# Kernel tuning notes

Hardware: AMD Instinct MI355X
Metric: run time of the kernel (lower is better)

## Reference

```python
import jax, jax.numpy as jnp
import numpy as np
from jax.scipy.special import logsumexp

B, S, H, T, M = 64, 512, 768, 500, 8
POSITION_WEIGHT = 0.6
LABEL_SMOOTH = 0.1
GAMMA = 2.0


def setup_inputs() -> dict:
    key = jax.random.key(0)
    ks = jax.random.split(key, 12)
    hidden = jax.random.normal(ks[0], (B, S, H), jnp.float32)  # BERT sequence_output stand-in
    lengths = jax.random.randint(ks[1], (B,), S // 2, S + 1)
    attention_mask = (jnp.arange(S)[None, :] < lengths[:, None]).astype(jnp.int32)
    position_labels = jax.random.randint(ks[2], (B, S), 0, 3).astype(jnp.int32)
    type_labels = jax.random.randint(ks[3], (B, M), 0, T).astype(jnp.int32)
    starts = jax.random.randint(ks[4], (B, M), 1, S // 2)
    ends = starts + jax.random.randint(ks[5], (B, M), 2, 8)
    valid = jax.random.uniform(ks[6], (B, M)) < 0.8  # some (batch, span) slots unused, like the original sum()>0 filter
    target_positions = jnp.where(valid[..., None], jnp.stack([starts, ends], -1), 0).astype(jnp.int32)
    # CRF params exactly as hardcoded in __init__
    trans = jnp.array([[-5.0, 20.0, -10000.0], [-50.0, 0.0, 50.0], [0.0, -50.0, 30.0]], jnp.float32)
    start_trans = jnp.array([0.0, 0.0, -10000.0], jnp.float32)
    end_trans = jnp.array([0.0, -100.0, 0.0], jnp.float32)
    return {
        'hidden': hidden,
        'attention_mask': attention_mask,
        'position_labels': position_labels,
        'type_labels': type_labels,
        'target_positions': target_positions,
        'bi_label_weight': jnp.asarray(0.5, jnp.float32),
        'W_pos': 0.02 * jax.random.normal(ks[7], (H, 3), jnp.float32),
        'b_pos': jnp.zeros((3,), jnp.float32),
        'start_trans': start_trans,
        'end_trans': end_trans,
        'trans': trans,
        'att_W1': 0.02 * jax.random.normal(ks[8], (H, 64), jnp.float32),
        'att_b1': jnp.zeros((64,), jnp.float32),
        'att_W2': 0.02 * jax.random.normal(ks[9], (64, 1), jnp.float32),
        'att_b2': jnp.zeros((1,), jnp.float32),
        'W_type': 0.02 * jax.random.normal(ks[10], (H, T), jnp.float32),
        'b_type': jnp.zeros((T,), jnp.float32),
    }


def crf_nll(em, labels, mask, start_trans, end_trans, trans):
    # torchcrf-style masked negative log-likelihood, reduction='none'
    maskf = mask.astype(em.dtype)
    emit = jnp.take_along_axis(em, labels[..., None], -1)[..., 0]  # [B,S]
    emit_score = (emit * maskf).sum(1)
    tr = trans[labels[:, :-1], labels[:, 1:]]  # [B,S-1]
    tr_score = (tr * maskf[:, 1:]).sum(1)
    last = mask.sum(1) - 1
    last_tags = jnp.take_along_axis(labels, last[:, None], 1)[:, 0]
    score = start_trans[labels[:, 0]] + emit_score + tr_score + end_trans[last_tags]
    # log partition via scan over time
    alpha = start_trans[None, :] + em[:, 0]  # [B,3]
    def step(alpha, xs):
        em_t, m_t = xs
        nxt = logsumexp(alpha[:, :, None] + trans[None, :, :] + em_t[:, None, :], axis=1)
        return jnp.where(m_t[:, None], nxt, alpha), None
    alpha, _ = jax.lax.scan(step, alpha, (em[:, 1:].transpose(1, 0, 2), mask[:, 1:].T))
    logZ = logsumexp(alpha + end_trans[None, :], axis=-1)
    return logZ - score  # = -log_likelihood


def reference(hidden, attention_mask, position_labels, type_labels, target_positions,
              bi_label_weight, W_pos, b_pos, start_trans, end_trans, trans,
              att_W1, att_b1, att_W2, att_b2, W_type, b_type):
    mask = attention_mask.astype(bool)
    emissions = hidden @ W_pos + b_pos  # [B,S,3]
    w = jnp.where(position_labels > 0, 1.0 + bi_label_weight, 1.0)[..., None]
    em_w = emissions * w
    position_loss = crf_nll(em_w, position_labels, mask, start_trans, end_trans, trans).mean()

    # span attention pooling, batched over all (B,M) pairs instead of the Python loop
    scores = (jnp.tanh(hidden @ att_W1 + att_b1) @ att_W2 + att_b2)[..., 0]  # [B,S]
    starts = target_positions[..., 0]
    ends = target_positions[..., 1]
    valid = target_positions.sum(-1) > 0  # [B,M]
    pos = jnp.arange(hidden.shape[1])
    span_mask = (pos[None, None, :] >= starts[..., None]) & (pos[None, None, :] < ends[..., None])  # [B,M,S]
    att = jnp.where(span_mask, scores[:, None, :], -1e9)
    aw = jax.nn.softmax(att, axis=-1)  # per-span softmax == softmax over the gathered span
    pooled = jnp.einsum('bms,bsh->bmh', aw, hidden)  # [B,M,H]
    logits = pooled @ W_type + b_type  # [B,M,T]

    # label-smoothed focal loss over valid spans only
    nT = logits.shape[-1]
    onehot = jax.nn.one_hot(type_labels, nT, dtype=logits.dtype)
    smooth = onehot * (1.0 - LABEL_SMOOTH) + LABEL_SMOOTH / nT
    logp = jax.nn.log_softmax(logits, axis=-1)
    probs = jnp.exp(logp)
    ce = -(smooth * logp).sum(-1)
    pt = (smooth * probs).sum(-1)
    focal = ce * (1.0 - pt) ** GAMMA
    v = valid.astype(focal.dtype)
    type_loss = (focal * v).sum() / jnp.maximum(v.sum(), 1.0) * 10.0

    joint = POSITION_WEIGHT * position_loss + (1.0 - POSITION_WEIGHT) * type_loss
    return jnp.stack([joint, position_loss, type_loss])
```

## Files before the change

### kernel.cpp

```cpp
#include <hip/hip_runtime.h>

#define L2E 1.44269504088896340736f
#define LN2 0.69314718055994530942f
#define NEGB -1e30f

typedef float f32x4 __attribute__((ext_vector_type(4)));
typedef __bf16 bf16x8 __attribute__((ext_vector_type(8)));

static constexpr int NB = 64, NS = 512, NH = 768, NT = 500, NM = 8;

static constexpr size_t WT_ALL_OFF   = 0;
static constexpr size_t WT_TYPE_OFF  = 122880;
static constexpr size_t EM_T_OFF     = 909312;
static constexpr size_t SCORES_OFF   = 1302528;
static constexpr size_t LABELS_T_OFF = 1433600;
static constexpr size_t LEN_OFF      = 1564672;
static constexpr size_t SCAL_OFF     = 3399936;
static constexpr size_t MATM_OFF     = 3400192;
static constexpr size_t PSC_OFF      = 3547648;

__device__ __forceinline__ unsigned short f2bf(float f) {
  unsigned u = __builtin_bit_cast(unsigned, f);
  u += 0x7FFFu + ((u >> 16) & 1u);
  return (unsigned short)(u >> 16);
}
__device__ __forceinline__ float sel3(float a, float b, float c, int i) {
  return i == 0 ? a : (i == 1 ? b : c);
}
__device__ __forceinline__ float lse3(float x, float y, float z) {
  float m = fmaxf(fmaxf(x, y), z);
  float p = exp2f((x - m) * L2E) + exp2f((y - m) * L2E) + exp2f((z - m) * L2E);
  return m + log2f(p) * LN2;
}
__device__ __forceinline__ int swz(int row, int slot) {
  return row * 128 + ((slot ^ (row & 7)) << 4);
}

__global__ __launch_bounds__(256) void ka_prep(
    const float* __restrict__ W1, const float* __restrict__ Wpos,
    const float* __restrict__ Wtype, const int* __restrict__ amask,
    unsigned short* __restrict__ wt_all, unsigned short* __restrict__ wt_type,
    int* __restrict__ lengths, float* __restrict__ scal) {
  const int bid = blockIdx.x, t = threadIdx.x;
  if (bid < 108) {
    __shared__ float tl[64][65];
    const bool is_type = bid < 96;
    const int kt = is_type ? (bid % 12) : (bid - 96);
    const int k0 = kt * 64;
    const int n0 = is_type ? (bid / 12) * 64 : 0;
    const int ld = is_type ? 500 : 64;
    const int nlim = is_type ? 500 : 64;
    const float* src = is_type ? Wtype : W1;
    unsigned short* dst = is_type ? wt_type : wt_all;
    const int n = t & 63;
    #pragma unroll
    for (int i = 0; i < 16; ++i) {
      int k = i * 4 + (t >> 6);
      tl[k][n] = (n0 + n < nlim) ? src[(size_t)(k0 + k) * ld + n0 + n] : 0.f;
    }
    __syncthreads();
    const int k = t & 63;
    #pragma unroll
    for (int i = 0; i < 16; ++i) {
      int nn = i * 4 + (t >> 6);
      dst[(size_t)(n0 + nn) * 768 + k0 + k] = f2bf(tl[k][nn]);
    }
  } else if (bid == 108) {
    for (int idx = t; idx < 16 * 768; idx += 256) {
      int n = 64 + idx / 768, k = idx % 768;
      float v = (n < 67) ? Wpos[k * 3 + (n - 64)] : 0.f;
      wt_all[(size_t)n * 768 + k] = f2bf(v);
    }
  } else {
    __shared__ int part[256];
    int bb = t >> 2, qq = t & 3;
    const int4* mp = (const int4*)(amask + bb * 512 + qq * 128);
    int s = 0;
    #pragma unroll 8
    for (int i = 0; i < 32; ++i) { int4 v = mp[i]; s += v.x + v.y + v.z + v.w; }
    part[t] = s;
    __syncthreads();
    if (qq == 0) lengths[bb] = part[t] + part[t + 1] + part[t + 2] + part[t + 3];
    if (t == 0) { scal[1] = 0.f; scal[2] = 0.f; }
  }
}

__global__ __launch_bounds__(256) void k1_gemm(
    const float* __restrict__ hidden, const int* __restrict__ plab,
    const float* __restrict__ bpos, const float* __restrict__ b1,
    const float* __restrict__ W2, const float* __restrict__ b2,
    const float* __restrict__ biw, const unsigned short* __restrict__ wt_all,
    float* __restrict__ em_t, float* __restrict__ scores, int* __restrict__ labels_t) {
  __shared__ char lds[8192 + 10240];
  char* As = lds;
  char* Bs = lds + 8192;
  const int t = threadIdx.x, w = t >> 6, l = t & 63;
  const int row0 = blockIdx.x * 64;

  f32x4 acc[5];
  #pragma unroll
  for (int nt = 0; nt < 5; ++nt) acc[nt] = (f32x4){0.f, 0.f, 0.f, 0.f};

  auto loadAB = [&](int it, float4 av[4], uint4 bv[3]) {
    const int k0 = it * 64;
    #pragma unroll
    for (int u = 0; u < 4; ++u) {
      int f4 = t + 256 * u, r = f4 >> 4, k4 = f4 & 15;
      av[u] = *(const float4*)(hidden + (size_t)(row0 + r) * 768 + k0 + 4 * k4);
    }
    bv[0] = *(const uint4*)(wt_all + (t >> 3) * 768 + k0 + 8 * (t & 7));
    bv[1] = *(const uint4*)(wt_all + ((t + 256) >> 3) * 768 + k0 + 8 * (t & 7));
    bv[2] = (t < 128) ? *(const uint4*)(wt_all + ((t + 512) >> 3) * 768 + k0 + 8 * (t & 7))
                      : (uint4){0, 0, 0, 0};
  };

  float4 avc[4]; uint4 bvc[3];
  loadAB(0, avc, bvc);

  for (int it = 0; it < 12; ++it) {
    __syncthreads();
    #pragma unroll
    for (int u = 0; u < 4; ++u) {
      int f4 = t + 256 * u, r = f4 >> 4, k4 = f4 & 15;
      unsigned lo = (unsigned)f2bf(avc[u].x) | ((unsigned)f2bf(avc[u].y) << 16);
      unsigned hi = (unsigned)f2bf(avc[u].z) | ((unsigned)f2bf(avc[u].w) << 16);
      int byte = r * 128 + (((k4 >> 1) ^ (r & 7)) << 4) + (k4 & 1) * 8;
      *(uint2*)(As + byte) = make_uint2(lo, hi);
    }
    { int n = t >> 3, kc = t & 7;         *(uint4*)(Bs + swz(n, kc)) = bvc[0]; }
    { int n = (t + 256) >> 3, kc = t & 7; *(uint4*)(Bs + swz(n, kc)) = bvc[1]; }
    if (t < 128) { int n = (t + 512) >> 3, kc = t & 7; *(uint4*)(Bs + swz(n, kc)) = bvc[2]; }
    __syncthreads();

    float4 avn[4]; uint4 bvn[3];
    if (it < 11) loadAB(it + 1, avn, bvn);

    #pragma unroll
    for (int ks = 0; ks < 2; ++ks) {
      int arow = 16 * w + (l & 15);
      int slot = 4 * ks + (l >> 4);
      bf16x8 a = *(const bf16x8*)(As + swz(arow, slot));
      #pragma unroll
      for (int nt = 0; nt < 5; ++nt) {
        int brow = 16 * nt + (l & 15);
        bf16x8 b = *(const bf16x8*)(Bs + swz(brow, slot));
        acc[nt] = __builtin_amdgcn_mfma_f32_16x16x32_bf16(a, b, acc[nt], 0, 0, 0);
      }
    }
    if (it < 11) {
      #pragma unroll
      for (int u = 0; u < 4; ++u) avc[u] = avn[u];
      #pragma unroll
      for (int u = 0; u < 3; ++u) bvc[u] = bvn[u];
    }
  }

  const int q = l >> 4, c16 = l & 15;
  const float bias2 = b2[0];
  #pragma unroll
  for (int r = 0; r < 4; ++r) {
    float s = 0.f;
    #pragma unroll
    for (int nt = 0; nt < 4; ++nt) {
      int c = 16 * nt + c16;
      float x = acc[nt][r] + b1[c];
      float th = 1.f - 2.f / (1.f + exp2f(x * (2.f * L2E)));
      s += th * W2[c];
    }
    #pragma unroll
    for (int off = 1; off < 16; off <<= 1) s += __shfl_xor(s, off, 64);
    if (c16 == 0) {
      int row = row0 + 16 * w + 4 * q + r;
      scores[row] = s + bias2;
    }
  }
  if (c16 < 3) {
    const float bi = biw[0];
    #pragma unroll
    for (int r = 0; r < 4; ++r) {
      int row = row0 + 16 * w + 4 * q + r;
      int bb = row >> 9, ss = row & 511;
      int lab = plab[row];
      float wgt = (lab > 0) ? 1.f + bi : 1.f;
      float ev = (acc[4][r] + bpos[c16]) * wgt;
      em_t[(ss * 3 + c16) * 64 + bb] = ev;
      if (c16 == 0) labels_t[ss * 64 + bb] = lab;
    }
  }
}

__global__ __launch_bounds__(64) void k2a_chunk(
    const float* __restrict__ em_t, const int* __restrict__ labels_t,
    const int* __restrict__ lengths, const float* __restrict__ trans,
    float* __restrict__ matM, float* __restrict__ psc) {
  const int b = threadIdx.x, c = blockIdx.x;
  float T0 = trans[0], T1 = trans[1], T2 = trans[2];
  float T3 = trans[3], T4 = trans[4], T5 = trans[5];
  float T6 = trans[6], T7 = trans[7], T8 = trans[8];
  const int L = lengths[b];
  const int s0 = 8 * c;
  int labp = labels_t[(c ? (s0 - 1) : 0) * 64 + b];

  float E0[8], E1[8], E2[8]; int LB[8];
  #pragma unroll
  for (int i = 0; i < 8; ++i) {
    E0[i] = em_t[((s0 + i) * 3 + 0) * 64 + b];
    E1[i] = em_t[((s0 + i) * 3 + 1) * 64 + b];
    E2[i] = em_t[((s0 + i) * 3 + 2) * 64 + b];
    LB[i] = labels_t[(s0 + i) * 64 + b];
  }

  float M[9];
  #pragma unroll
  for (int i = 0; i < 9; ++i) M[i] = (i == 0 || i == 4 || i == 8) ? 0.f : NEGB;
  float sc = 0.f;

  #pragma unroll
  for (int i = 0; i < 8; ++i) {
    int s = s0 + i;
    bool act = (s >= 1) && (s < L);
    float N[9];
    #pragma unroll
    for (int r = 0; r < 3; ++r) {
      float ma = M[3 * r], mb = M[3 * r + 1], mc = M[3 * r + 2];
      N[3 * r + 0] = lse3(ma + T0, mb + T3, mc + T6) + E0[i];
      N[3 * r + 1] = lse3(ma + T1, mb + T4, mc + T7) + E1[i];
      N[3 * r + 2] = lse3(ma + T2, mb + T5, mc + T8) + E2[i];
    }
    #pragma unroll
    for (int r = 0; r < 9; ++r) M[r] = act ? N[r] : M[r];
    int lab = LB[i];
    float ev = sel3(E0[i], E1[i], E2[i], lab);
    float trv = sel3(sel3(T0, T1, T2, lab),
                     sel3(T3, T4, T5, lab),
                     sel3(T6, T7, T8, lab), labp);
    sc += act ? (ev + trv) : 0.f;
    labp = lab;
  }
  #pragma unroll
  for (int i = 0; i < 9; ++i) matM[(c * 9 + i) * 64 + b] = M[i];
  psc[c * 64 + b] = sc;
}

__global__ __launch_bounds__(256) void kd_pool_gemm_focal(
    const float* __restrict__ hidden, const float* __restrict__ scores,
    const int* __restrict__ tpos, const int* __restrict__ tlab,
    const unsigned short* __restrict__ wt_type, const float* __restrict__ btype,
    float* __restrict__ scal) {
  __shared__ unsigned short Apool[8][776];
  __shared__ float red[4][8][3];
  __shared__ float vl[8];
  const int t = threadIdx.x, w = t >> 6, l = t & 63;
  const int b = blockIdx.x;

  {
    const int sp = t >> 5;
    const int span = b * 8 + sp;
    const int st = tpos[span * 2], en = tpos[span * 2 + 1];
    const int len = (st + en > 0) ? (en - st) : 0;
    float sv[7], aw[7];
    float wm = -1e30f;
    #pragma unroll
    for (int j = 0; j < 7; ++j) {
      sv[j] = (j < len) ? scores[b * 512 + st + j] : -1e30f;
      wm = fmaxf(wm, sv[j]);
    }
    float den = 0.f;
    #pragma unroll
    for (int j = 0; j < 7; ++j) {
      aw[j] = (j < len) ? exp2f((sv[j] - wm) * L2E) : 0.f;
      den += aw[j];
    }
    float inv = (den > 0.f) ? 1.f / den : 0.f;
    #pragma unroll
    for (int j = 0; j < 7; ++j) aw[j] *= inv;

    const int h0 = (t & 31) * 24;
    float ap[24];
    #pragma unroll
    for (int i = 0; i < 24; ++i) ap[i] = 0.f;
    #pragma unroll
    for (int j = 0; j < 7; ++j) {
      if (j < len) {
        const float4* hp = (const float4*)(hidden + (size_t)(b * 512 + st + j) * 768 + h0);
        #pragma unroll
        for (int i = 0; i < 6; ++i) {
          float4 v = hp[i];
          ap[4 * i + 0] += aw[j] * v.x; ap[4 * i + 1] += aw[j] * v.y;
          ap[4 * i + 2] += aw[j] * v.z; ap[4 * i + 3] += aw[j] * v.w;
        }
      }
    }
    unsigned short* dp = &Apool[sp][h0];
    #pragma unroll
    for (int g = 0; g < 3; ++g) {
      uint4 v;
      v.x = (unsigned)f2bf(ap[8 * g + 0]) | ((unsigned)f2bf(ap[8 * g + 1]) << 16);
      v.y = (unsigned)f2bf(ap[8 * g + 2]) | ((unsigned)f2bf(ap[8 * g + 3]) << 16);
      v.z = (unsigned)f2bf(ap[8 * g + 4]) | ((unsigned)f2bf(ap[8 * g + 5]) << 16);
      v.w = (unsigned)f2bf(ap[8 * g + 6]) | ((unsigned)f2bf(ap[8 * g + 7]) << 16);
      *(uint4*)(dp + 8 * g) = v;
    }
  }
  __syncthreads();

  f32x4 acc[8];
  #pragma unroll
  for (int nt = 0; nt < 8; ++nt) acc[nt] = (f32x4){0.f, 0.f, 0.f, 0.f};
  const int arow = l & 15;
  const bf16x8 zerov = (bf16x8)(__bf16)0.f;
  for (int ks = 0; ks < 24; ++ks) {
    bf16x8 a = (arow < 8) ? *(const bf16x8*)(&Apool[arow][ks * 32 + 8 * (l >> 4)]) : zerov;
    #pragma unroll
    for (int nt = 0; nt < 8; ++nt) {
      int col = 128 * w + 16 * nt + (l & 15);
      bf16x8 bb = *(const bf16x8*)(wt_type + (size_t)col * 768 + ks * 32 + 8 * (l >> 4));
      acc[nt] = __builtin_amdgcn_mfma_f32_16x16x32_bf16(a, bb, acc[nt], 0, 0, 0);
    }
  }

  float bt[8]; bool vc[8];
  #pragma unroll
  for (int nt = 0; nt < 8; ++nt) {
    int col = 128 * w + 16 * nt + (l & 15);
    vc[nt] = col < 500;
    bt[nt] = vc[nt] ? btype[col] : 0.f;
  }
  #pragma unroll
  for (int r = 0; r < 4; ++r) {
    float lmax = -1e30f, ssum = 0.f;
    #pragma unroll
    for (int nt = 0; nt < 8; ++nt) {
      float lv = vc[nt] ? (acc[nt][r] + bt[nt]) : -1e30f;
      lmax = fmaxf(lmax, lv);
      ssum += vc[nt] ? lv : 0.f;
    }
    #pragma unroll
    for (int off = 1; off < 16; off <<= 1) lmax = fmaxf(lmax, __shfl_xor(lmax, off, 64));
    float sexp = 0.f;
    #pragma unroll
    for (int nt = 0; nt < 8; ++nt) {
      float lv = vc[nt] ? (acc[nt][r] + bt[nt]) : -1e30f;
      sexp += vc[nt] ? exp2f((lv - lmax) * L2E) : 0.f;
    }
    #pragma unroll
    for (int off = 1; off < 16; off <<= 1) {
      sexp += __shfl_xor(sexp, off, 64);
      ssum += __shfl_xor(ssum, off, 64);
    }
    if ((l & 15) == 0 && (l >> 4) < 2) {
      int row = 4 * (l >> 4) + r;
      red[w][row][0] = lmax; red[w][row][1] = sexp; red[w][row][2] = ssum;
    }
    if ((l >> 4) < 2) {
      int row = 4 * (l >> 4) + r;
      int lbl = tlab[b * 8 + row];
      if ((lbl >> 7) == w && (lbl & 15) == (l & 15)) {
        #pragma unroll
        for (int nt = 0; nt < 8; ++nt)
          if (((lbl >> 4) & 7) == nt) vl[row] = acc[nt][r] + btype[lbl];
      }
    }
  }
  __syncthreads();

  float fv = 0.f, vv = 0.f;
  if (t < 8) {
    const int row = t;
    float gm = fmaxf(fmaxf(red[0][row][0], red[1][row][0]),
                     fmaxf(red[2][row][0], red[3][row][0]));
    float sexp = 0.f, ssum = 0.f;
    #pragma unroll
    for (int i = 0; i < 4; ++i) {
      sexp += red[i][row][1] * exp2f((red[i][row][0] - gm) * L2E);
      ssum += red[i][row][2];
    }
    float logZ = gm + log2f(sexp) * LN2;
    float lp = vl[row] - logZ;
    float ce = -(0.9f * lp + 2e-4f * (ssum - 500.f * logZ));
    float pt = 0.9f * exp2f(lp * L2E) + 2e-4f;
    float focal = ce * (1.f - pt) * (1.f - pt);
    int span = b * 8 + row;
    bool valid = (tpos[span * 2] + tpos[span * 2 + 1]) > 0;
    fv = valid ? focal : 0.f;
    vv = valid ? 1.f : 0.f;
  }
  #pragma unroll
  for (int off = 1; off < 8; off <<= 1) {
    fv += __shfl_xor(fv, off, 64);
    vv += __shfl_xor(vv, off, 64);
  }
  if (t == 0) {
    atomicAdd(&scal[1], fv);
    atomicAdd(&scal[2], vv);
  }
}

__global__ __launch_bounds__(64) void k_final(
    const float* __restrict__ em_t, const int* __restrict__ labels_t,
    const int* __restrict__ lengths, const float* __restrict__ strans,
    const float* __restrict__ etrans, const float* __restrict__ matM,
    const float* __restrict__ psc, const float* __restrict__ scal,
    float* __restrict__ out) {
  const int b = threadIdx.x;
  const int L = lengths[b];
  const float st0 = strans[0], st1 = strans[1], st2 = strans[2];
  const float et0 = etrans[0], et1 = etrans[1], et2 = etrans[2];
  float e00 = em_t[0 * 64 + b], e01 = em_t[1 * 64 + b], e02 = em_t[2 * 64 + b];
  int lab0 = labels_t[b];
  float a0 = st0 + e00, a1 = st1 + e01, a2 = st2 + e02;
  float score = sel3(st0, st1, st2, lab0) + sel3(e00, e01, e02, lab0);

  float cur[4][10];
  #pragma unroll
  for (int j = 0; j < 4; ++j) {
    #pragma unroll
    for (int i = 0; i < 9; ++i) cur[j][i] = matM[(j * 9 + i) * 64 + b];
    cur[j][9] = psc[j * 64 + b];
  }

  for (int r = 0; r < 16; ++r) {
    float nxt[4][10];
    if (r < 15) {
      #pragma unroll
      for (int j = 0; j < 4; ++j) {
        int c = (r + 1) * 4 + j;
        #pragma unroll
        for (int i = 0; i < 9; ++i) nxt[j][i] = matM[(c * 9 + i) * 64 + b];
        nxt[j][9] = psc[c * 64 + b];
      }
    }
    #pragma unroll
    for (int j = 0; j < 4; ++j) {
      float n0 = lse3(a0 + cur[j][0], a1 + cur[j][3], a2 + cur[j][6]);
      float n1 = lse3(a0 + cur[j][1], a1 + cur[j][4], a2 + cur[j][7]);
      float n2 = lse3(a0 + cur[j][2], a1 + cur[j][5], a2 + cur[j][8]);
      a0 = n0; a1 = n1; a2 = n2;
      score += cur[j][9];
    }
    if (r < 15) {
      #pragma unroll
      for (int j = 0; j < 4; ++j)
        #pragma unroll
        for (int i = 0; i < 10; ++i) cur[j][i] = nxt[j][i];
    }
  }

  int last = labels_t[(L - 1) * 64 + b];
  score += sel3(et0, et1, et2, last);
  float logZ = lse3(a0 + et0, a1 + et1, a2 + et2);
  float nll = logZ - score;
  #pragma unroll
  for (int off = 1; off < 64; off <<= 1) nll += __shfl_xor(nll, off, 64);
  if (b == 0) {
    float pos = nll / 64.f;
    float type = scal[1] / fmaxf(scal[2], 1.f) * 10.f;
    out[0] = 0.6f * pos + 0.4f * type;
    out[1] = pos;
    out[2] = type;
  }
}

extern "C" void kernel_launch(void* const* d_in, const int* in_sizes, int n_in,
                              void* d_out, int out_size, void* d_ws, size_t ws_size,
                              hipStream_t stream) {
  const float* hidden = (const float*)d_in[0];
  const int*   amask  = (const int*)d_in[1];
  const int*   plab   = (const int*)d_in[2];
  const int*   tlab   = (const int*)d_in[3];
  const int*   tpos   = (const int*)d_in[4];
  const float* biw    = (const float*)d_in[5];
  const float* Wpos   = (const float*)d_in[6];
  const float* bpos   = (const float*)d_in[7];
  const float* strans = (const float*)d_in[8];
  const float* etrans = (const float*)d_in[9];
  const float* trans  = (const float*)d_in[10];
  const float* W1     = (const float*)d_in[11];
  const float* b1     = (const float*)d_in[12];
  const float* W2     = (const float*)d_in[13];
  const float* b2     = (const float*)d_in[14];
  const float* Wtype  = (const float*)d_in[15];
  const float* btype  = (const float*)d_in[16];
  float* out = (float*)d_out;
  char* ws = (char*)d_ws;

  unsigned short* wt_all  = (unsigned short*)(ws + WT_ALL_OFF);
  unsigned short* wt_type = (unsigned short*)(ws + WT_TYPE_OFF);
  float* em_t    = (float*)(ws + EM_T_OFF);
  float* scores  = (float*)(ws + SCORES_OFF);
  int*   labelsT = (int*)(ws + LABELS_T_OFF);
  int*   lengths = (int*)(ws + LEN_OFF);
  float* scal    = (float*)(ws + SCAL_OFF);
  float* matM    = (float*)(ws + MATM_OFF);
  float* psc     = (float*)(ws + PSC_OFF);

  ka_prep<<<110, 256, 0, stream>>>(W1, Wpos, Wtype, amask, wt_all, wt_type, lengths, scal);
  k1_gemm<<<512, 256, 0, stream>>>(hidden, plab, bpos, b1, W2, b2, biw, wt_all,
                                   em_t, scores, labelsT);
  k2a_chunk<<<64, 64, 0, stream>>>(em_t, labelsT, lengths, trans, matM, psc);
  kd_pool_gemm_focal<<<64, 256, 0, stream>>>(hidden, scores, tpos, tlab, wt_type, btype, scal);
  k_final<<<1, 64, 0, stream>>>(em_t, labelsT, lengths, strans, etrans, matM, psc, scal, out);
}
```

Baseline: 104.2 us.

## Drop LDS staging in projection GEMM and fuse CRF chunk with pooling kernel

The hidden-state projection GEMM no longer stages A and B tiles through shared memory with barriers. Each lane now loads its MFMA fragments straight from global memory, converting fp32 to bf16 in registers. Separately, the CRF chunk kernel and the span-pooling/focal kernel are merged into one launch of 80 blocks, with 16 extra blocks running the CRF chunks four waves each, which removes one kernel launch and lets the two run concurrently. The direct global loads give up the LDS data sharing across waves and the prefetch of the next tile, so weight fragments are re-read per wave and latency may be less hidden.

```diff
diff --git a/kernel.cpp b/kernel.cpp
--- a/kernel.cpp
+++ b/kernel.cpp
@@ -32,8 +32,13 @@
   float p = exp2f((x - m) * L2E) + exp2f((y - m) * L2E) + exp2f((z - m) * L2E);
   return m + log2f(p) * LN2;
 }
-__device__ __forceinline__ int swz(int row, int slot) {
-  return row * 128 + ((slot ^ (row & 7)) << 4);
+__device__ __forceinline__ bf16x8 pack8(float4 lo, float4 hi) {
+  union { unsigned u[4]; bf16x8 v; } r;
+  r.u[0] = (unsigned)f2bf(lo.x) | ((unsigned)f2bf(lo.y) << 16);
+  r.u[1] = (unsigned)f2bf(lo.z) | ((unsigned)f2bf(lo.w) << 16);
+  r.u[2] = (unsigned)f2bf(hi.x) | ((unsigned)f2bf(hi.y) << 16);
+  r.u[3] = (unsigned)f2bf(hi.z) | ((unsigned)f2bf(hi.w) << 16);
+  return r.v;
 }
 
 __global__ __launch_bounds__(256) void ka_prep(
@@ -91,71 +96,41 @@
     const float* __restrict__ W2, const float* __restrict__ b2,
     const float* __restrict__ biw, const unsigned short* __restrict__ wt_all,
     float* __restrict__ em_t, float* __restrict__ scores, int* __restrict__ labels_t) {
-  __shared__ char lds[8192 + 10240];
-  char* As = lds;
-  char* Bs = lds + 8192;
   const int t = threadIdx.x, w = t >> 6, l = t & 63;
   const int row0 = blockIdx.x * 64;
+  const int c16 = l & 15, q = l >> 4;
+  const float* aptr = hidden + (size_t)(row0 + 16 * w + c16) * 768;
 
   f32x4 acc[5];
   #pragma unroll
   for (int nt = 0; nt < 5; ++nt) acc[nt] = (f32x4){0.f, 0.f, 0.f, 0.f};
 
-  auto loadAB = [&](int it, float4 av[4], uint4 bv[3]) {
+  #pragma unroll 2
+  for (int it = 0; it < 12; ++it) {
     const int k0 = it * 64;
-    #pragma unroll
-    for (int u = 0; u < 4; ++u) {
-      int f4 = t + 256 * u, r = f4 >> 4, k4 = f4 & 15;
-      av[u] = *(const float4*)(hidden + (size_t)(row0 + r) * 768 + k0 + 4 * k4);
-    }
-    bv[0] = *(const uint4*)(wt_all + (t >> 3) * 768 + k0 + 8 * (t & 7));
-    bv[1] = *(const uint4*)(wt_all + ((t + 256) >> 3) * 768 + k0 + 8 * (t & 7));
-    bv[2] = (t < 128) ? *(const uint4*)(wt_all + ((t + 512) >> 3) * 768 + k0 + 8 * (t & 7))
-                      : (uint4){0, 0, 0, 0};
-  };
-
-  float4 avc[4]; uint4 bvc[3];
-  loadAB(0, avc, bvc);
-
-  for (int it = 0; it < 12; ++it) {
-    __syncthreads();
-    #pragma unroll
-    for (int u = 0; u < 4; ++u) {
-      int f4 = t + 256 * u, r = f4 >> 4, k4 = f4 & 15;
-      unsigned lo = (unsigned)f2bf(avc[u].x) | ((unsigned)f2bf(avc[u].y) << 16);
-      unsigned hi = (unsigned)f2bf(avc[u].z) | ((unsigned)f2bf(avc[u].w) << 16);
-      int byte = r * 128 + (((k4 >> 1) ^ (r & 7)) << 4) + (k4 & 1) * 8;
-      *(uint2*)(As + byte) = make_uint2(lo, hi);
-    }
-    { int n = t >> 3, kc = t & 7;         *(uint4*)(Bs + swz(n, kc)) = bvc[0]; }
-    { int n = (t + 256) >> 3, kc = t & 7; *(uint4*)(Bs + swz(n, kc)) = bvc[1]; }
-    if (t < 128) { int n = (t + 512) >> 3, kc = t & 7; *(uint4*)(Bs + swz(n, kc)) = bvc[2]; }
-    __syncthreads();
-
-    float4 avn[4]; uint4 bvn[3];
-    if (it < 11) loadAB(it + 1, avn, bvn);
-
-    #pragma unroll
-    for (int ks = 0; ks < 2; ++ks) {
-      int arow = 16 * w + (l & 15);
-      int slot = 4 * ks + (l >> 4);
-      bf16x8 a = *(const bf16x8*)(As + swz(arow, slot));
-      #pragma unroll
-      for (int nt = 0; nt < 5; ++nt) {
-        int brow = 16 * nt + (l & 15);
-        bf16x8 b = *(const bf16x8*)(Bs + swz(brow, slot));
-        acc[nt] = __builtin_amdgcn_mfma_f32_16x16x32_bf16(a, b, acc[nt], 0, 0, 0);
-      }
-    }
-    if (it < 11) {
-      #pragma unroll
-      for (int u = 0; u < 4; ++u) avc[u] = avn[u];
-      #pragma unroll
-      for (int u = 0; u < 3; ++u) bvc[u] = bvn[u];
-    }
-  }
-
-  const int q = l >> 4, c16 = l & 15;
+    const int ka0 = k0 + q * 8;
+    const int ka1 = k0 + (4 + q) * 8;
+    float4 a0lo = *(const float4*)(aptr + ka0);
+    float4 a0hi = *(const float4*)(aptr + ka0 + 4);
+    float4 a1lo = *(const float4*)(aptr + ka1);
+    float4 a1hi = *(const float4*)(aptr + ka1 + 4);
+    bf16x8 bf[2][5];
+    #pragma unroll
+    for (int nt = 0; nt < 5; ++nt) {
+      const unsigned short* bp = wt_all + (size_t)(16 * nt + c16) * 768;
+      bf[0][nt] = *(const bf16x8*)(bp + ka0);
+      bf[1][nt] = *(const bf16x8*)(bp + ka1);
+    }
+    bf16x8 a0 = pack8(a0lo, a0hi);
+    bf16x8 a1 = pack8(a1lo, a1hi);
+    #pragma unroll
+    for (int nt = 0; nt < 5; ++nt)
+      acc[nt] = __builtin_amdgcn_mfma_f32_16x16x32_bf16(a0, bf[0][nt], acc[nt], 0, 0, 0);
+    #pragma unroll
+    for (int nt = 0; nt < 5; ++nt)
+      acc[nt] = __builtin_amdgcn_mfma_f32_16x16x32_bf16(a1, bf[1][nt], acc[nt], 0, 0, 0);
+  }
+
   const float bias2 = b2[0];
   #pragma unroll
   for (int r = 0; r < 4; ++r) {
@@ -189,69 +164,71 @@
   }
 }
 
-__global__ __launch_bounds__(64) void k2a_chunk(
-    const float* __restrict__ em_t, const int* __restrict__ labels_t,
-    const int* __restrict__ lengths, const float* __restrict__ trans,
-    float* __restrict__ matM, float* __restrict__ psc) {
-  const int b = threadIdx.x, c = blockIdx.x;
-  float T0 = trans[0], T1 = trans[1], T2 = trans[2];
-  float T3 = trans[3], T4 = trans[4], T5 = trans[5];
-  float T6 = trans[6], T7 = trans[7], T8 = trans[8];
-  const int L = lengths[b];
-  const int s0 = 8 * c;
-  int labp = labels_t[(c ? (s0 - 1) : 0) * 64 + b];
-
-  float E0[8], E1[8], E2[8]; int LB[8];
-  #pragma unroll
-  for (int i = 0; i < 8; ++i) {
-    E0[i] = em_t[((s0 + i) * 3 + 0) * 64 + b];
-    E1[i] = em_t[((s0 + i) * 3 + 1) * 64 + b];
-    E2[i] = em_t[((s0 + i) * 3 + 2) * 64 + b];
-    LB[i] = labels_t[(s0 + i) * 64 + b];
-  }
-
-  float M[9];
-  #pragma unroll
-  for (int i = 0; i < 9; ++i) M[i] = (i == 0 || i == 4 || i == 8) ? 0.f : NEGB;
-  float sc = 0.f;
-
-  #pragma unroll
-  for (int i = 0; i < 8; ++i) {
-    int s = s0 + i;
-    bool act = (s >= 1) && (s < L);
-    float N[9];
-    #pragma unroll
-    for (int r = 0; r < 3; ++r) {
-      float ma = M[3 * r], mb = M[3 * r + 1], mc = M[3 * r + 2];
-      N[3 * r + 0] = lse3(ma + T0, mb + T3, mc + T6) + E0[i];
-      N[3 * r + 1] = lse3(ma + T1, mb + T4, mc + T7) + E1[i];
-      N[3 * r + 2] = lse3(ma + T2, mb + T5, mc + T8) + E2[i];
-    }
-    #pragma unroll
-    for (int r = 0; r < 9; ++r) M[r] = act ? N[r] : M[r];
-    int lab = LB[i];
-    float ev = sel3(E0[i], E1[i], E2[i], lab);
-    float trv = sel3(sel3(T0, T1, T2, lab),
-                     sel3(T3, T4, T5, lab),
-                     sel3(T6, T7, T8, lab), labp);
-    sc += act ? (ev + trv) : 0.f;
-    labp = lab;
-  }
-  #pragma unroll
-  for (int i = 0; i < 9; ++i) matM[(c * 9 + i) * 64 + b] = M[i];
-  psc[c * 64 + b] = sc;
-}
-
-__global__ __launch_bounds__(256) void kd_pool_gemm_focal(
+__global__ __launch_bounds__(256) void kf_fused(
     const float* __restrict__ hidden, const float* __restrict__ scores,
     const int* __restrict__ tpos, const int* __restrict__ tlab,
     const unsigned short* __restrict__ wt_type, const float* __restrict__ btype,
-    float* __restrict__ scal) {
+    const float* __restrict__ em_t, const int* __restrict__ labels_t,
+    const int* __restrict__ lengths, const float* __restrict__ trans,
+    float* __restrict__ matM, float* __restrict__ psc, float* __restrict__ scal) {
+  const int bid = blockIdx.x;
+  const int t = threadIdx.x, w = t >> 6, l = t & 63;
+
+  if (bid >= 64) {
+    const int b = l, c = (bid - 64) * 4 + w;
+    float T0 = trans[0], T1 = trans[1], T2 = trans[2];
+    float T3 = trans[3], T4 = trans[4], T5 = trans[5];
+    float T6 = trans[6], T7 = trans[7], T8 = trans[8];
+    const int L = lengths[b];
+    const int s0 = 8 * c;
+    int labp = labels_t[(c ? (s0 - 1) : 0) * 64 + b];
+
+    float E0[8], E1[8], E2[8]; int LB[8];
+    #pragma unroll
+    for (int i = 0; i < 8; ++i) {
+      E0[i] = em_t[((s0 + i) * 3 + 0) * 64 + b];
+      E1[i] = em_t[((s0 + i) * 3 + 1) * 64 + b];
+      E2[i] = em_t[((s0 + i) * 3 + 2) * 64 + b];
+      LB[i] = labels_t[(s0 + i) * 64 + b];
+    }
+
+    float M[9];
+    #pragma unroll
+    for (int i = 0; i < 9; ++i) M[i] = (i == 0 || i == 4 || i == 8) ? 0.f : NEGB;
+    float sc = 0.f;
+
+    #pragma unroll
+    for (int i = 0; i < 8; ++i) {
+      int s = s0 + i;
+      bool act = (s >= 1) && (s < L);
+      float N[9];
+      #pragma unroll
+      for (int r = 0; r < 3; ++r) {
+        float ma = M[3 * r], mb = M[3 * r + 1], mc = M[3 * r + 2];
+        N[3 * r + 0] = lse3(ma + T0, mb + T3, mc + T6) + E0[i];
+        N[3 * r + 1] = lse3(ma + T1, mb + T4, mc + T7) + E1[i];
+        N[3 * r + 2] = lse3(ma + T2, mb + T5, mc + T8) + E2[i];
+      }
+      #pragma unroll
+      for (int r = 0; r < 9; ++r) M[r] = act ? N[r] : M[r];
+      int lab = LB[i];
+      float ev = sel3(E0[i], E1[i], E2[i], lab);
+      float trv = sel3(sel3(T0, T1, T2, lab),
+                       sel3(T3, T4, T5, lab),
+                       sel3(T6, T7, T8, lab), labp);
+      sc += act ? (ev + trv) : 0.f;
+      labp = lab;
+    }
+    #pragma unroll
+    for (int i = 0; i < 9; ++i) matM[(c * 9 + i) * 64 + b] = M[i];
+    psc[c * 64 + b] = sc;
+    return;
+  }
+
   __shared__ unsigned short Apool[8][776];
   __shared__ float red[4][8][3];
   __shared__ float vl[8];
-  const int t = threadIdx.x, w = t >> 6, l = t & 63;
-  const int b = blockIdx.x;
+  const int b = bid;
 
   {
     const int sp = t >> 5;
@@ -497,7 +474,7 @@
   ka_prep<<<110, 256, 0, stream>>>(W1, Wpos, Wtype, amask, wt_all, wt_type, lengths, scal);
   k1_gemm<<<512, 256, 0, stream>>>(hidden, plab, bpos, b1, W2, b2, biw, wt_all,
                                    em_t, scores, labelsT);
-  k2a_chunk<<<64, 64, 0, stream>>>(em_t, labelsT, lengths, trans, matM, psc);
-  kd_pool_gemm_focal<<<64, 256, 0, stream>>>(hidden, scores, tpos, tlab, wt_type, btype, scal);
+  kf_fused<<<80, 256, 0, stream>>>(hidden, scores, tpos, tlab, wt_type, btype,
+                                   em_t, labelsT, lengths, trans, matM, psc, scal);
   k_final<<<1, 64, 0, stream>>>(em_t, labelsT, lengths, strans, etrans, matM, psc, scal, out);
 }
```

New measurement: 112.1 us. +7.6%, slower.
